# Kernel tuning notes

Measured on AMD Instinct MI355X. Metric: run time of the kernel, lower is better.

## Reference

```python
import jax, jax.numpy as jnp
import numpy as np

B, H, W, C = 16, 64, 64, 256
HEADS, WS, SHIFTS, QD = 8, 8, (0, 4), 512
N = WS * WS
HD = C // HEADS
MLP_H = 4 * C
DEPTH = 2
EPS = 1e-5


def _rel_pos_index():
    coords = np.stack(np.meshgrid(np.arange(WS), np.arange(WS), indexing='ij'))  # [2,ws,ws]
    flat = coords.reshape(2, -1)
    rel = (flat[:, :, None] - flat[:, None, :]).transpose(1, 2, 0)  # [N,N,2]
    rel[..., 0] += WS - 1
    rel[..., 1] += WS - 1
    rel[..., 0] *= 2 * WS - 1
    return jnp.asarray(rel.sum(-1))  # [N,N] int


def _shift_mask(shift):
    img = np.zeros((H, W))
    cnt = 0
    for hs in (slice(0, -WS), slice(-WS, -shift), slice(-shift, None)):
        for ws_ in (slice(0, -WS), slice(-WS, -shift), slice(-shift, None)):
            img[hs, ws_] = cnt
            cnt += 1
    mw = img.reshape(H // WS, WS, W // WS, WS).transpose(0, 2, 1, 3).reshape(-1, N)  # [nW,N]
    am = mw[:, None, :] - mw[:, :, None]
    return jnp.asarray(np.where(am != 0, -100.0, 0.0).astype(np.float32))  # [nW,N,N]


RPI = _rel_pos_index()


def layernorm(x, g, b):
    mu = x.mean(-1, keepdims=True)
    var = ((x - mu) ** 2).mean(-1, keepdims=True)
    return (x - mu) * jax.lax.rsqrt(var + EPS) * g + b


def window_partition(x):  # [B,H,W,C] -> [B*nW, N, C]
    x = x.reshape(B, H // WS, WS, W // WS, WS, C)
    return x.transpose(0, 1, 3, 2, 4, 5).reshape(-1, N, C)


def window_reverse(w):  # [B*nW, N, C] -> [B,H,W,C]
    x = w.reshape(B, H // WS, W // WS, WS, WS, C)
    return x.transpose(0, 1, 3, 2, 4, 5).reshape(B, H, W, C)


def swin_block(x, shift, n1g, n1b, qkvw, qkvb, rpb, pw, pb, n2g, n2b, f1w, f1b, f2w, f2b):
    shortcut = x
    y = layernorm(x, n1g, n1b).reshape(B, H, W, C)
    if shift > 0:
        y = jnp.roll(y, (-shift, -shift), axis=(1, 2))
    xw = window_partition(y)                                      # [B_, N, C]
    qkv = (xw @ qkvw + qkvb).reshape(-1, N, 3, HEADS, HD)
    q, k, v = (qkv[:, :, i].transpose(0, 2, 1, 3) for i in range(3))  # [B_,h,N,hd]
    scores = jnp.einsum('bhnd,bhmd->bhnm', q * (HD ** -0.5), k)
    bias = rpb[RPI].transpose(2, 0, 1)                            # [h,N,N]
    scores = scores + bias[None]
    if shift > 0:
        mask = _shift_mask(shift)                                 # [nW,N,N]
        nW = mask.shape[0]
        scores = scores.reshape(B, nW, HEADS, N, N) + mask[None, :, None]
        scores = scores.reshape(-1, HEADS, N, N)
    attn = jax.nn.softmax(scores, axis=-1)
    out = jnp.einsum('bhnm,bhmd->bhnd', attn, v).transpose(0, 2, 1, 3).reshape(-1, N, C)
    out = out @ pw + pb
    y = window_reverse(out)
    if shift > 0:
        y = jnp.roll(y, (shift, shift), axis=(1, 2))
    x = shortcut + y.reshape(B, H * W, C)
    h = layernorm(x, n2g, n2b)
    h = jax.nn.gelu(h @ f1w + f1b, approximate=False) @ f2w + f2b
    return x + h


def cross_attn(x, cond, cng, cnb, inw, inb, outw, outb):
    xn = layernorm(x, cng, cnb)
    q = xn @ inw[:C].T + inb[:C]
    k = cond @ inw[C:2 * C].T + inb[C:2 * C]
    v = cond @ inw[2 * C:].T + inb[2 * C:]
    Tq, Tk = q.shape[1], k.shape[1]
    q = q.reshape(B, Tq, HEADS, HD).transpose(0, 2, 1, 3) * (HD ** -0.5)
    k = k.reshape(B, Tk, HEADS, HD).transpose(0, 2, 1, 3)
    v = v.reshape(B, Tk, HEADS, HD).transpose(0, 2, 1, 3)
    a = jax.nn.softmax(jnp.einsum('bhqd,bhkd->bhqk', q, k), axis=-1)
    o = jnp.einsum('bhqk,bhkd->bhqd', a, v).transpose(0, 2, 1, 3).reshape(B, Tq, C)
    return x + o @ outw.T + outb


def setup_inputs() -> dict:
    key = jax.random.key(0)
    ks = iter(jax.random.split(key, 40))
    s = 0.02
    d = {
        'x': jax.random.normal(next(ks), (B, H * W, C), jnp.float32),
        'emb': jax.random.normal(next(ks), (B, 1, QD), jnp.float32),
        'qenc_w': jax.random.normal(next(ks), (QD, C)) * s,
        'qenc_b': jnp.zeros((C,)),
        'n1_g': jnp.ones((DEPTH, C)), 'n1_b': jnp.zeros((DEPTH, C)),
        'qkv_w': jax.random.normal(next(ks), (DEPTH, C, 3 * C)) * s,
        'qkv_b': jnp.zeros((DEPTH, 3 * C)),
        'rpb': jax.random.normal(next(ks), (DEPTH, (2 * WS - 1) ** 2, HEADS)) * s,
        'proj_w': jax.random.normal(next(ks), (DEPTH, C, C)) * s,
        'proj_b': jnp.zeros((DEPTH, C)),
        'n2_g': jnp.ones((DEPTH, C)), 'n2_b': jnp.zeros((DEPTH, C)),
        'fc1_w': jax.random.normal(next(ks), (DEPTH, C, MLP_H)) * s,
        'fc1_b': jnp.zeros((DEPTH, MLP_H)),
        'fc2_w': jax.random.normal(next(ks), (DEPTH, MLP_H, C)) * s,
        'fc2_b': jnp.zeros((DEPTH, C)),
        'cn_g': jnp.ones((DEPTH, C)), 'cn_b': jnp.zeros((DEPTH, C)),
        'ca_in_w': jax.random.normal(next(ks), (DEPTH, 3 * C, C)) * s,
        'ca_in_b': jnp.zeros((DEPTH, 3 * C)),
        'ca_out_w': jax.random.normal(next(ks), (DEPTH, C, C)) * s,
        'ca_out_b': jnp.zeros((DEPTH, C)),
    }
    return d


def reference(x, emb, qenc_w, qenc_b, n1_g, n1_b, qkv_w, qkv_b, rpb, proj_w, proj_b,
              n2_g, n2_b, fc1_w, fc1_b, fc2_w, fc2_b, cn_g, cn_b,
              ca_in_w, ca_in_b, ca_out_w, ca_out_b):
    for d in range(DEPTH):
        x = swin_block(x, SHIFTS[d], n1_g[d], n1_b[d], qkv_w[d], qkv_b[d], rpb[d],
                       proj_w[d], proj_b[d], n2_g[d], n2_b[d],
                       fc1_w[d], fc1_b[d], fc2_w[d], fc2_b[d])
        cond = emb @ qenc_w + qenc_b  # recomputed per block as in original
        x = cross_attn(x, cond, cn_g[d], cn_b[d], ca_in_w[d], ca_in_b[d],
                       ca_out_w[d], ca_out_b[d])
    return x
```

## Files before the change

kernel.cpp:

```cpp
#include <hip/hip_runtime.h>


typedef unsigned short bfraw;
typedef short s16x8 __attribute__((ext_vector_type(8)));
typedef short s16x4 __attribute__((ext_vector_type(4)));
typedef float f32x4 __attribute__((ext_vector_type(4)));

#define DEV static __device__ __forceinline__

DEV float b2f(int u){
  union { unsigned int i; float f; } x;
  x.i = ((unsigned int)u & 0xffffu) << 16;
  return x.f;
}
DEV unsigned short f2bbits(float f){
  union { float f; unsigned int i; } x; x.f = f;
  unsigned int i = x.i;
  unsigned int lsb = (i >> 16) & 1u;
  i += 0x7fffu + lsb;
  return (unsigned short)(i >> 16);
}
DEV float gelu_tanh(float x){
  float t2 = 1.5957691216057308f * fmaf(0.044715f * x * x, x, x);
  float e = __expf(-t2);
  return x * __builtin_amdgcn_rcpf(1.f + e);
}

#define GLOAD_LDS16(g, l) __builtin_amdgcn_global_load_lds(                      \
    (const __attribute__((address_space(1))) void*)(g),                          \
    (__attribute__((address_space(3))) void*)(l), 16, 0, 0)

__global__ void k_tr(const float* __restrict__ in, bfraw* __restrict__ out, int K, int N){
  int idx = blockIdx.x * 256 + threadIdx.x;
  if (idx >= K * N) return;
  int n = idx / K, k = idx - n * K;
  out[idx] = f2bbits(in[(size_t)k * N + n]);
}

__global__ __launch_bounds__(256) void k_ln(
    const float* __restrict__ x, const float* __restrict__ g,
    const float* __restrict__ b, bfraw* __restrict__ y)
{
  const int lane = threadIdx.x & 63, wv = threadIdx.x >> 6;
  const size_t row = (size_t)blockIdx.x * 4 + wv;
  const float4 v = *(const float4*)(x + row * 256 + lane * 4);
  float s  = v.x + v.y + v.z + v.w;
  float s2 = v.x*v.x + v.y*v.y + v.z*v.z + v.w*v.w;
#pragma unroll
  for (int off = 32; off; off >>= 1){
    s  += __shfl_xor(s,  off);
    s2 += __shfl_xor(s2, off);
  }
  float mu  = s * (1.f/256.f);
  float var = s2 * (1.f/256.f) - mu * mu;
  float rs  = rsqrtf(var + 1e-5f);
  const float4 gv = *(const float4*)(g + lane * 4);
  const float4 bv = *(const float4*)(b + lane * 4);
  s16x4 o;
  o[0] = (short)f2bbits((v.x - mu) * rs * gv.x + bv.x);
  o[1] = (short)f2bbits((v.y - mu) * rs * gv.y + bv.y);
  o[2] = (short)f2bbits((v.z - mu) * rs * gv.z + bv.z);
  o[3] = (short)f2bbits((v.w - mu) * rs * gv.w + bv.w);
  *(s16x4*)(y + row * 256 + lane * 4) = o;
}

template<int EPI>
__global__ __launch_bounds__(256, 2) void k_gemm(
    const bfraw* __restrict__ A, const bfraw* __restrict__ Bt,
    const float* __restrict__ bias,
    bfraw* __restrict__ Cout, int ldc,
    float* __restrict__ xfp, const float* __restrict__ xin,
    const float* __restrict__ addv,
    int M, int N, int K, int shift)
{
  constexpr int BK = 64;
  __shared__ __align__(16) bfraw sA[128 * BK];
  __shared__ __align__(16) bfraw sB[128 * BK];
  const int tid = threadIdx.x, lane = tid & 63, w = tid >> 6;
  const int lo16 = lane & 15, hg = lane >> 4;
  const int nbm = M >> 7, nbn = N >> 7;
  const int nwg = nbm * nbn;
  const int bid = blockIdx.x;
  const int wgid = (bid & 7) * (nwg >> 3) + (bid >> 3);
  const int tn = wgid % nbn, tm = wgid / nbn;
  const int m0 = tm << 7, n0 = tn << 7;
  const int wm = w & 1, wn = w >> 1;
  f32x4 acc[4][4] = {};

  const int srow = (w << 5) + (lane >> 3);
  const int scol = (((lane & 7) ^ (lane >> 3)) << 3);
  const int ksw  = (lane & 7) << 3;
  const bfraw* gA = A  + (size_t)(m0 + srow) * K + scol;
  const bfraw* gB = Bt + (size_t)(n0 + srow) * K + scol;

  for (int kt = 0; kt < K; kt += BK){
    __syncthreads();
#pragma unroll
    for (int i = 0; i < 4; ++i){
      GLOAD_LDS16(gA + (size_t)(i * 8) * K + kt, &sA[(w * 4 + i) * 512]);
      GLOAD_LDS16(gB + (size_t)(i * 8) * K + kt, &sB[(w * 4 + i) * 512]);
    }
    __syncthreads();
#pragma unroll
    for (int ks = 0; ks < 2; ++ks){
      const int ko = (ks * 32 + (hg << 3)) ^ ksw;
      s16x8 af[4], bfr[4];
#pragma unroll
      for (int i = 0; i < 4; ++i){
        af[i]  = *(const s16x8*)&sA[((wm << 6) + (i << 4) + lo16) * BK + ko];
        bfr[i] = *(const s16x8*)&sB[((wn << 6) + (i << 4) + lo16) * BK + ko];
      }
#pragma unroll
      for (int ni = 0; ni < 4; ++ni)
#pragma unroll
        for (int mi = 0; mi < 4; ++mi)
          acc[ni][mi] = __builtin_amdgcn_mfma_f32_16x16x32_bf16(
              bfr[ni], af[mi], acc[ni][mi], 0, 0, 0);
    }
  }

  const int cb = n0 + (wn << 6) + 4 * hg;
  f32x4 bv4[4];
#pragma unroll
  for (int ni = 0; ni < 4; ++ni) bv4[ni] = *(const f32x4*)(bias + cb + ni * 16);

#pragma unroll
  for (int mi = 0; mi < 4; ++mi){
    const int r = m0 + (wm << 6) + (mi << 4) + lo16;
    if constexpr (EPI == 0 || EPI == 1){
      bfraw* crow = Cout + (size_t)r * ldc + cb;
#pragma unroll
      for (int ni = 0; ni < 4; ++ni){
        f32x4 v = acc[ni][mi] + bv4[ni];
        s16x4 o;
#pragma unroll
        for (int j = 0; j < 4; ++j){
          float val = v[j];
          if constexpr (EPI == 1) val = gelu_tanh(val);
          o[j] = (short)f2bbits(val);
        }
        *(s16x4*)(crow + ni * 16) = o;
      }
    } else if constexpr (EPI == 2){
      int b_ = r >> 12, rem = r & 4095;
      int wi = rem >> 6, n_ = rem & 63;
      int gi = ((wi >> 3) * 8 + (n_ >> 3) + shift) & 63;
      int gj = ((wi & 7) * 8 + (n_ & 7) + shift) & 63;
      size_t rowoff = ((size_t)b_ << 12) + gi * 64 + gj;
      const float* xi = xin + rowoff * 256 + cb;
      float*       xo = xfp + rowoff * 256 + cb;
#pragma unroll
      for (int ni = 0; ni < 4; ++ni){
        f32x4 v = acc[ni][mi] + bv4[ni] + *(const f32x4*)(xi + ni * 16);
        *(f32x4*)(xo + ni * 16) = v;
      }
    } else {
      const float* av = addv + (size_t)(r >> 12) * 256 + cb;
      float* xo = xfp + (size_t)r * 256 + cb;
#pragma unroll
      for (int ni = 0; ni < 4; ++ni){
        f32x4 v = acc[ni][mi] + bv4[ni] + *(const f32x4*)(xo + ni * 16)
                + *(const f32x4*)(av + ni * 16);
        *(f32x4*)(xo + ni * 16) = v;
      }
    }
  }
}

__global__ __launch_bounds__(64) void k_bias(const float* __restrict__ rpb,
                                             float* __restrict__ biasPk)
{
  const int blk = blockIdx.x;
  const int d = blk >> 5, cls = (blk >> 3) & 3, h = blk & 7;
  const int l = threadIdx.x, lo16 = l & 15, hg = l >> 4;
  const float* rp = rpb + (size_t)d * 225 * 8;
  float* ob = biasPk + (((size_t)d * 4 + cls) * 8 + h) * 4096;
#pragma unroll
  for (int mi = 0; mi < 4; ++mi)
#pragma unroll
    for (int ni = 0; ni < 4; ++ni)
#pragma unroll
      for (int j = 0; j < 4; ++j){
        int k = 16 * mi + 4 * hg + j, q = 16 * ni + lo16;
        int qr = q >> 3, qc = q & 7, kr = k >> 3, kc = k & 7;
        float v = rp[((qr - kr + 7) * 15 + (qc - kc + 7)) * 8 + h];
        if (d == 1){
          int lq = ((cls >> 1) ? (qr < 4 ? 1 : 2) : 0) * 3 + ((cls & 1) ? (qc < 4 ? 1 : 2) : 0);
          int lk = ((cls >> 1) ? (kr < 4 ? 1 : 2) : 0) * 3 + ((cls & 1) ? (kc < 4 ? 1 : 2) : 0);
          if (lq != lk) v -= 100.f;
        }
        ob[(mi * 4 + ni) * 256 + l * 4 + j] = v;
      }
}

__global__ __launch_bounds__(64) void k_attn(
    const bfraw* __restrict__ qkv, const float* __restrict__ biasPk,
    bfraw* __restrict__ aout, int shift)
{
  __shared__ __align__(16) bfraw sV[64 * 32];
  __shared__ __align__(16) bfraw sP[64 * 64];
  const int win = blockIdx.x >> 3, h = blockIdx.x & 7;
  const int b = win >> 6, wr = (win >> 3) & 7, wc = win & 7;
  const int l = threadIdx.x, lo16 = l & 15, hg = l >> 4;

  auto grow_of = [&](int n) -> size_t {
    int gi = (wr * 8 + (n >> 3) + shift) & 63;
    int gj = (wc * 8 + (n & 7) + shift) & 63;
    return ((size_t)b << 12) + gi * 64 + gj;
  };

  s16x8 vreg[4];
#pragma unroll
  for (int i = 0; i < 4; ++i){
    int row = i * 16 + (l >> 2);
    vreg[i] = *(const s16x8*)(qkv + grow_of(row) * 768 + 512 + h * 32 + (l & 3) * 8);
  }
#pragma unroll
  for (int i = 0; i < 4; ++i)
    *(s16x8*)&sV[i * 512 + l * 8] = vreg[i];

  s16x8 aK[4], bQ[4];
#pragma unroll
  for (int t = 0; t < 4; ++t){
    const bfraw* base = qkv + grow_of(16 * t + lo16) * 768 + h * 32 + hg * 8;
    bQ[t] = *(const s16x8*)base;
    aK[t] = *(const s16x8*)(base + 256);
  }

  f32x4 acc[4][4] = {};
#pragma unroll
  for (int mi = 0; mi < 4; ++mi)
#pragma unroll
    for (int ni = 0; ni < 4; ++ni)
      acc[mi][ni] = __builtin_amdgcn_mfma_f32_16x16x32_bf16(aK[mi], bQ[ni], acc[mi][ni], 0, 0, 0);

  const int cls = ((wr == 7) ? 2 : 0) | ((wc == 7) ? 1 : 0);
  const float* bb = biasPk + ((size_t)(cls * 8 + h)) * 4096;
#pragma unroll
  for (int mi = 0; mi < 4; ++mi)
#pragma unroll
    for (int ni = 0; ni < 4; ++ni){
      f32x4 bv4 = *(const f32x4*)(bb + (mi * 4 + ni) * 256 + l * 4);
      acc[mi][ni] = acc[mi][ni] * 0.17677669529663689f + bv4;
    }

#pragma unroll
  for (int ni = 0; ni < 4; ++ni){
    float m = acc[0][ni][0];
#pragma unroll
    for (int mi = 0; mi < 4; ++mi)
#pragma unroll
      for (int j = 0; j < 4; ++j) m = fmaxf(m, acc[mi][ni][j]);
    m = fmaxf(m, __shfl_xor(m, 16));
    m = fmaxf(m, __shfl_xor(m, 32));
    float s = 0.f;
#pragma unroll
    for (int mi = 0; mi < 4; ++mi)
#pragma unroll
      for (int j = 0; j < 4; ++j){
        float e = __expf(acc[mi][ni][j] - m);
        acc[mi][ni][j] = e; s += e;
      }
    s += __shfl_xor(s, 16);
    s += __shfl_xor(s, 32);
    float inv = 1.f / s;
#pragma unroll
    for (int mi = 0; mi < 4; ++mi)
#pragma unroll
      for (int j = 0; j < 4; ++j) acc[mi][ni][j] *= inv;
  }

#pragma unroll
  for (int mi = 0; mi < 4; ++mi)
#pragma unroll
    for (int ni = 0; ni < 4; ++ni){
      unsigned int w0, w1;
      asm("v_cvt_pk_bf16_f32 %0, %1, %2" : "=v"(w0) : "v"(acc[mi][ni][0]), "v"(acc[mi][ni][1]));
      asm("v_cvt_pk_bf16_f32 %0, %1, %2" : "=v"(w1) : "v"(acc[mi][ni][2]), "v"(acc[mi][ni][3]));
      int q = 16 * ni + lo16;
      int ad = (q * 128 + (16 * mi + 4 * hg) * 2) ^ ((q & 7) << 4);
      *(uint2*)((char*)sP + ad) = make_uint2(w0, w1);
    }

  asm volatile("s_waitcnt lgkmcnt(0)" ::: "memory");
  __builtin_amdgcn_sched_barrier(0);

  f32x4 opv[4][2] = {};
#pragma unroll
  for (int kt = 0; kt < 2; ++kt){
    s16x8 ap[4];
#pragma unroll
    for (int qi = 0; qi < 4; ++qi){
      int q = 16 * qi + lo16;
      int ad = (q * 128 + (kt * 32 + hg * 8) * 2) ^ ((q & 7) << 4);
      ap[qi] = *(const s16x8*)((const char*)sP + ad);
    }
    s16x8 vb[2];
#pragma unroll
    for (int nt = 0; nt < 2; ++nt)
#pragma unroll
      for (int e = 0; e < 8; ++e)
        vb[nt][e] = (short)sV[(kt * 32 + hg * 8 + e) * 32 + nt * 16 + lo16];
#pragma unroll
    for (int qi = 0; qi < 4; ++qi)
#pragma unroll
      for (int nt = 0; nt < 2; ++nt)
        opv[qi][nt] = __builtin_amdgcn_mfma_f32_16x16x32_bf16(ap[qi], vb[nt], opv[qi][nt], 0, 0, 0);
  }

  bfraw* ob = aout + ((size_t)win * 64) * 256 + h * 32 + lo16;
#pragma unroll
  for (int qi = 0; qi < 4; ++qi)
#pragma unroll
    for (int nt = 0; nt < 2; ++nt)
#pragma unroll
      for (int j = 0; j < 4; ++j)
        ob[(size_t)(16 * qi + 4 * hg + j) * 256 + nt * 16] = f2bbits(opv[qi][nt][j]);
}

__global__ __launch_bounds__(256) void k_addvec(
    const float* __restrict__ emb, const float* __restrict__ qw, const float* __restrict__ qb,
    const float* __restrict__ inw, const float* __restrict__ inb,
    const float* __restrict__ outw, const float* __restrict__ outb,
    float* __restrict__ addv)
{
  const int d = blockIdx.x >> 4, b = blockIdx.x & 15;
  const int j = threadIdx.x;
  __shared__ float sc[256], sv[256];
  float a = qb[j];
  for (int k = 0; k < 512; ++k) a = fmaf(emb[b * 512 + k], qw[k * 256 + j], a);
  sc[j] = a; __syncthreads();
  float v = inb[d * 768 + 512 + j];
  const float* wrp = inw + (size_t)d * 768 * 256 + (size_t)(512 + j) * 256;
  for (int k = 0; k < 256; ++k) v = fmaf(sc[k], wrp[k], v);
  sv[j] = v; __syncthreads();
  float o = outb[d * 256 + j];
  const float* wop = outw + (size_t)d * 65536 + (size_t)j * 256;
  for (int k = 0; k < 256; ++k) o = fmaf(sv[k], wop[k], o);
  addv[(size_t)(d * 16 + b) * 256 + j] = o;
}

extern "C" void kernel_launch(void* const* d_in, const int* in_sizes, int n_in,
                              void* d_out, int out_size, void* d_ws, size_t ws_size,
                              hipStream_t stream)
{
  (void)in_sizes; (void)n_in; (void)out_size; (void)ws_size;
  const float* x_in     = (const float*)d_in[0];
  const float* emb      = (const float*)d_in[1];
  const float* qenc_w   = (const float*)d_in[2];
  const float* qenc_b   = (const float*)d_in[3];
  const float* n1_g     = (const float*)d_in[4];
  const float* n1_b     = (const float*)d_in[5];
  const float* qkv_w    = (const float*)d_in[6];
  const float* qkv_b    = (const float*)d_in[7];
  const float* rpb      = (const float*)d_in[8];
  const float* proj_w   = (const float*)d_in[9];
  const float* proj_b   = (const float*)d_in[10];
  const float* n2_g     = (const float*)d_in[11];
  const float* n2_b     = (const float*)d_in[12];
  const float* fc1_w    = (const float*)d_in[13];
  const float* fc1_b    = (const float*)d_in[14];
  const float* fc2_w    = (const float*)d_in[15];
  const float* fc2_b    = (const float*)d_in[16];
  const float* ca_in_w  = (const float*)d_in[19];
  const float* ca_in_b  = (const float*)d_in[20];
  const float* ca_out_w = (const float*)d_in[21];
  const float* ca_out_b = (const float*)d_in[22];

  float* xfp  = (float*)d_out;
  char* ws = (char*)d_ws;
  bfraw* ybuf = (bfraw*)ws;
  bfraw* qkvb = (bfraw*)(ws + ((size_t)32 << 20));
  bfraw* wT   = (bfraw*)(ws + ((size_t)160 << 20));
  float* biasPk = (float*)(ws + ((size_t)166 << 20));

  bfraw *qkvT[2], *projT[2], *fc1T[2], *fc2T[2];
  size_t off = 0;
  for (int d = 0; d < 2; ++d){ qkvT[d] = wT + off; off += 768 * 256; }
  for (int d = 0; d < 2; ++d){ projT[d] = wT + off; off += 256 * 256; }
  for (int d = 0; d < 2; ++d){ fc1T[d] = wT + off; off += 1024 * 256; }
  for (int d = 0; d < 2; ++d){ fc2T[d] = wT + off; off += 256 * 1024; }
  float* addv = (float*)(wT + ((off + 1) & ~(size_t)1));

  for (int d = 0; d < 2; ++d){
    k_tr<<<(256 * 768  + 255) / 256, 256, 0, stream>>>(qkv_w  + (size_t)d * 256 * 768,  qkvT[d], 256, 768);
    k_tr<<<(256 * 256  + 255) / 256, 256, 0, stream>>>(proj_w + (size_t)d * 256 * 256,  projT[d], 256, 256);
    k_tr<<<(256 * 1024 + 255) / 256, 256, 0, stream>>>(fc1_w  + (size_t)d * 256 * 1024, fc1T[d], 256, 1024);
    k_tr<<<(1024 * 256 + 255) / 256, 256, 0, stream>>>(fc2_w  + (size_t)d * 1024 * 256, fc2T[d], 1024, 256);
  }
  k_bias<<<64, 64, 0, stream>>>(rpb, biasPk);
  k_addvec<<<32, 256, 0, stream>>>(emb, qenc_w, qenc_b, ca_in_w, ca_in_b, ca_out_w, ca_out_b, addv);

  for (int d = 0; d < 2; ++d){
    const int shift = d ? 4 : 0;
    const float* resid_in = d ? (const float*)xfp : x_in;
    k_ln<<<16384, 256, 0, stream>>>(resid_in, n1_g + d * 256, n1_b + d * 256, ybuf);
    k_gemm<0><<<512 * 6, 256, 0, stream>>>(ybuf, qkvT[d], qkv_b + d * 768, qkvb, 768,
                                           nullptr, nullptr, nullptr, 65536, 768, 256, 0);
    k_attn<<<8192, 64, 0, stream>>>(qkvb, biasPk + (size_t)d * 4 * 8 * 4096, ybuf, shift);
    k_gemm<2><<<512 * 2, 256, 0, stream>>>(ybuf, projT[d], proj_b + d * 256, nullptr, 0,
                                           xfp, resid_in, nullptr, 65536, 256, 256, shift);
    k_ln<<<16384, 256, 0, stream>>>(xfp, n2_g + d * 256, n2_b + d * 256, ybuf);
    k_gemm<1><<<512 * 8, 256, 0, stream>>>(ybuf, fc1T[d], fc1_b + d * 1024, qkvb, 1024,
                                           nullptr, nullptr, nullptr, 65536, 1024, 256, 0);
    k_gemm<3><<<512 * 2, 256, 0, stream>>>(qkvb, fc2T[d], fc2_b + d * 256, nullptr, 0,
                                           xfp, nullptr, addv + (size_t)d * 16 * 256,
                                           65536, 256, 1024, 0);
  }
}
```

Baseline: 686.2 us.

## Double-buffer GEMM LDS tiles and prefetch residual epilogue operands before main loop

The GEMM kernel now keeps two LDS buffers for the A and B tiles. It issues the global-to-LDS loads for the next K tile before computing on the current one, which cuts the barriers per iteration from two to one. The fused-residual epilogues now load their residual and broadcast-add inputs (and compute the shifted row mapping) before the K loop, so that latency is hidden behind the MFMA work. The cost is double the LDS per block and about 64 more live VGPRs held across the loop, which could lower occupancy or cause spills.

```diff
diff --git a/kernel.cpp b/kernel.cpp
--- a/kernel.cpp
+++ b/kernel.cpp
@@ -74,8 +74,8 @@
     int M, int N, int K, int shift)
 {
   constexpr int BK = 64;
-  __shared__ __align__(16) bfraw sA[128 * BK];
-  __shared__ __align__(16) bfraw sB[128 * BK];
+  __shared__ __align__(16) bfraw sA[2][128 * BK];
+  __shared__ __align__(16) bfraw sB[2][128 * BK];
   const int tid = threadIdx.x, lane = tid & 63, w = tid >> 6;
   const int lo16 = lane & 15, hg = lane >> 4;
   const int nbm = M >> 7, nbn = N >> 7;
@@ -93,22 +93,63 @@
   const bfraw* gA = A  + (size_t)(m0 + srow) * K + scol;
   const bfraw* gB = Bt + (size_t)(n0 + srow) * K + scol;
 
-  for (int kt = 0; kt < K; kt += BK){
+  const int cb = n0 + (wn << 6) + 4 * hg;
+
+  f32x4 bv4[4];
+#pragma unroll
+  for (int ni = 0; ni < 4; ++ni) bv4[ni] = *(const f32x4*)(bias + cb + ni * 16);
+  size_t rowoff_[4];
+  f32x4 pre[16], pav[4];
+  if constexpr (EPI == 2 || EPI == 3){
+#pragma unroll
+    for (int mi = 0; mi < 4; ++mi){
+      const int r = m0 + (wm << 6) + (mi << 4) + lo16;
+      if constexpr (EPI == 2){
+        int b_ = r >> 12, rem = r & 4095;
+        int wi = rem >> 6, n_ = rem & 63;
+        int gi = ((wi >> 3) * 8 + (n_ >> 3) + shift) & 63;
+        int gj = ((wi & 7) * 8 + (n_ & 7) + shift) & 63;
+        rowoff_[mi] = ((size_t)b_ << 12) + gi * 64 + gj;
+      } else {
+        rowoff_[mi] = (size_t)r;
+      }
+      const float* src = (EPI == 2 ? xin : (const float*)xfp) + rowoff_[mi] * 256 + cb;
+#pragma unroll
+      for (int ni = 0; ni < 4; ++ni)
+        pre[mi * 4 + ni] = *(const f32x4*)(src + ni * 16);
+    }
+    if constexpr (EPI == 3){
+      const float* av = addv + (size_t)(m0 >> 12) * 256 + cb;
+#pragma unroll
+      for (int ni = 0; ni < 4; ++ni) pav[ni] = *(const f32x4*)(av + ni * 16);
+    }
+  }
+
+  const int nt = K / BK;
+#pragma unroll
+  for (int i = 0; i < 4; ++i){
+    GLOAD_LDS16(gA + (size_t)(i * 8) * K, &sA[0][(w * 4 + i) * 512]);
+    GLOAD_LDS16(gB + (size_t)(i * 8) * K, &sB[0][(w * 4 + i) * 512]);
+  }
+  for (int t = 0; t < nt; ++t){
     __syncthreads();
-#pragma unroll
-    for (int i = 0; i < 4; ++i){
-      GLOAD_LDS16(gA + (size_t)(i * 8) * K + kt, &sA[(w * 4 + i) * 512]);
-      GLOAD_LDS16(gB + (size_t)(i * 8) * K + kt, &sB[(w * 4 + i) * 512]);
-    }
-    __syncthreads();
+    const int cur = t & 1;
+    if (t + 1 < nt){
+      const int nxt = cur ^ 1, kt = (t + 1) * BK;
+#pragma unroll
+      for (int i = 0; i < 4; ++i){
+        GLOAD_LDS16(gA + (size_t)(i * 8) * K + kt, &sA[nxt][(w * 4 + i) * 512]);
+        GLOAD_LDS16(gB + (size_t)(i * 8) * K + kt, &sB[nxt][(w * 4 + i) * 512]);
+      }
+    }
 #pragma unroll
     for (int ks = 0; ks < 2; ++ks){
       const int ko = (ks * 32 + (hg << 3)) ^ ksw;
       s16x8 af[4], bfr[4];
 #pragma unroll
       for (int i = 0; i < 4; ++i){
-        af[i]  = *(const s16x8*)&sA[((wm << 6) + (i << 4) + lo16) * BK + ko];
-        bfr[i] = *(const s16x8*)&sB[((wn << 6) + (i << 4) + lo16) * BK + ko];
+        af[i]  = *(const s16x8*)&sA[cur][((wm << 6) + (i << 4) + lo16) * BK + ko];
+        bfr[i] = *(const s16x8*)&sB[cur][((wn << 6) + (i << 4) + lo16) * BK + ko];
       }
 #pragma unroll
       for (int ni = 0; ni < 4; ++ni)
@@ -119,15 +160,10 @@
     }
   }
 
-  const int cb = n0 + (wn << 6) + 4 * hg;
-  f32x4 bv4[4];
-#pragma unroll
-  for (int ni = 0; ni < 4; ++ni) bv4[ni] = *(const f32x4*)(bias + cb + ni * 16);
-
 #pragma unroll
   for (int mi = 0; mi < 4; ++mi){
-    const int r = m0 + (wm << 6) + (mi << 4) + lo16;
     if constexpr (EPI == 0 || EPI == 1){
+      const int r = m0 + (wm << 6) + (mi << 4) + lo16;
       bfraw* crow = Cout + (size_t)r * ldc + cb;
 #pragma unroll
       for (int ni = 0; ni < 4; ++ni){
@@ -142,27 +178,15 @@
         *(s16x4*)(crow + ni * 16) = o;
       }
     } else if constexpr (EPI == 2){
-      int b_ = r >> 12, rem = r & 4095;
-      int wi = rem >> 6, n_ = rem & 63;
-      int gi = ((wi >> 3) * 8 + (n_ >> 3) + shift) & 63;
-      int gj = ((wi & 7) * 8 + (n_ & 7) + shift) & 63;
-      size_t rowoff = ((size_t)b_ << 12) + gi * 64 + gj;
-      const float* xi = xin + rowoff * 256 + cb;
-      float*       xo = xfp + rowoff * 256 + cb;
-#pragma unroll
-      for (int ni = 0; ni < 4; ++ni){
-        f32x4 v = acc[ni][mi] + bv4[ni] + *(const f32x4*)(xi + ni * 16);
-        *(f32x4*)(xo + ni * 16) = v;
-      }
+      float* xo = xfp + rowoff_[mi] * 256 + cb;
+#pragma unroll
+      for (int ni = 0; ni < 4; ++ni)
+        *(f32x4*)(xo + ni * 16) = acc[ni][mi] + bv4[ni] + pre[mi * 4 + ni];
     } else {
-      const float* av = addv + (size_t)(r >> 12) * 256 + cb;
-      float* xo = xfp + (size_t)r * 256 + cb;
-#pragma unroll
-      for (int ni = 0; ni < 4; ++ni){
-        f32x4 v = acc[ni][mi] + bv4[ni] + *(const f32x4*)(xo + ni * 16)
-                + *(const f32x4*)(av + ni * 16);
-        *(f32x4*)(xo + ni * 16) = v;
-      }
+      float* xo = xfp + rowoff_[mi] * 256 + cb;
+#pragma unroll
+      for (int ni = 0; ni < 4; ++ni)
+        *(f32x4*)(xo + ni * 16) = acc[ni][mi] + bv4[ni] + pre[mi * 4 + ni] + pav[ni];
     }
   }
 }
```

Result: no change. 689.3 us (+0.5%).
